# Kernel tuning notes

Measured on AMD Instinct MI355X. Metric: run time of the kernel, lower is better.

The kernel has to match this reference:

```python
import jax, jax.numpy as jnp
import numpy as np

K = 10
BN_EPS = 1e-5


def _edgeconv(x, W, b, gamma, beta):
    """DGCNN EdgeConv: kNN on x, edge feat [x_i, x_j - x_i], Linear->(BN)->ReLU, max over k.
    x: [N, C]; W: [2C, Cout]; gamma/beta: [Cout] or None."""
    sq = jnp.sum(x * x, axis=1)                      # [N]
    dist = sq[:, None] + sq[None, :] - 2.0 * (x @ x.T)  # [N, N] squared dists
    _, idx = jax.lax.top_k(-dist, K)                 # [N, K] (includes self)
    xj = x[idx]                                      # [N, K, C] gather
    xi = jnp.broadcast_to(x[:, None, :], xj.shape)   # [N, K, C]
    e = jnp.concatenate([xi, xj - xi], axis=-1)      # [N, K, 2C]
    h = e @ W + b                                    # [N, K, Cout]
    if gamma is not None:                            # BatchNorm1d (training-mode batch stats)
        mu = h.mean(axis=(0, 1))
        var = h.var(axis=(0, 1))
        h = (h - mu) * jax.lax.rsqrt(var + BN_EPS) * gamma + beta
    h = jax.nn.relu(h)
    return h.max(axis=1)                             # [N, Cout]


def _aggregate(f, seg_ids, num_segments):
    return jax.ops.segment_max(f, seg_ids, num_segments=num_segments)


def setup_inputs() -> dict:
    key = jax.random.key(0)
    ks = jax.random.split(key, 12)
    N, B = 16384, 64
    x = jax.random.normal(ks[0], (N, 3), dtype=jnp.float32)
    n_pts = jnp.full((B,), N // B, dtype=jnp.int32)

    def lin(k, fi, fo):
        s = 1.0 / np.sqrt(fi)
        kw, kb = jax.random.split(k)
        return (jax.random.uniform(kw, (fi, fo), jnp.float32, -s, s),
                jax.random.uniform(kb, (fo,), jnp.float32, -s, s))

    W1, b1 = lin(ks[1], 6, 64)
    W2, b2 = lin(ks[2], 128, 64)
    W3, b3 = lin(ks[3], 128, 64)
    W4, b4 = lin(ks[4], 128, 64)
    Wp, bp = lin(ks[5], 256, 128)
    g1 = jnp.ones((64,), jnp.float32); be1 = jnp.zeros((64,), jnp.float32)
    g3 = jnp.ones((64,), jnp.float32); be3 = jnp.zeros((64,), jnp.float32)
    return {"x": x, "n_pts": n_pts,
            "W1": W1, "b1": b1, "g1": g1, "be1": be1,
            "W2": W2, "b2": b2,
            "W3": W3, "b3": b3, "g3": g3, "be3": be3,
            "W4": W4, "b4": b4,
            "Wp": Wp, "bp": bp}


def reference(x, n_pts, W1, b1, g1, be1, W2, b2, W3, b3, g3, be3, W4, b4, Wp, bp):
    N = x.shape[0]
    B = n_pts.shape[0]
    seg_ids = jnp.repeat(jnp.arange(B, dtype=jnp.int32), n_pts, total_repeat_length=N)

    f1 = _edgeconv(x,  W1, b1, g1,  be1)   # [N, 64]
    f2 = _edgeconv(f1, W2, b2, None, None)
    f3 = _edgeconv(f2, W3, b3, g3,  be3)
    f4 = _edgeconv(f3, W4, b4, None, None)

    p = jnp.concatenate([_aggregate(f, seg_ids, B) for f in (f1, f2, f3, f4)], axis=1)  # [B, 256]
    f = jnp.tanh(p @ Wp + bp)              # [B, 128]
    f = f / (jnp.linalg.norm(f, axis=1, keepdims=True) + 1e-9)
    return f
```

## Files before the change

### kernel.cpp

```cpp
#include <hip/hip_runtime.h>
#include <hip/hip_bf16.h>

constexpr int N = 16384;
constexpr int KNN = 10;
constexpr int CF = 64;
constexpr int NS64 = 12;
constexpr int NS3 = 12;

#define FBIG 1e30f

typedef __attribute__((ext_vector_type(8))) __bf16 bfv8;
typedef __attribute__((ext_vector_type(4))) float f32x4;

#define TOPK_INSERT(dval, jval)                                            \
  if ((dval) < bmax) {                                                     \
    float mv = bd[0]; int slot = 0;                                        \
    _Pragma("unroll") for (int s_ = 1; s_ < 10; ++s_)                      \
      if (bd[s_] > mv) { mv = bd[s_]; slot = s_; }                         \
    _Pragma("unroll") for (int s_ = 0; s_ < 10; ++s_)                      \
      if (slot == s_) { bd[s_] = (dval); bi[s_] = (jval); }                \
    bmax = bd[0];                                                          \
    _Pragma("unroll") for (int s_ = 1; s_ < 10; ++s_)                      \
      bmax = fmaxf(bmax, bd[s_]);                                          \
  }

__device__ inline ushort bf16_rne(float x) {
  unsigned u = __float_as_uint(x);
  return (ushort)((u + 0x7FFFu + ((u >> 16) & 1u)) >> 16);
}
__device__ inline float bf16_to_f(ushort h) { return __uint_as_float(((unsigned)h) << 16); }

__global__ __launch_bounds__(256) void pack3_kernel(const float* __restrict__ X,
                                                    float4* __restrict__ xp,
                                                    int* __restrict__ gtauI,
                                                    float* __restrict__ accum) {
  int i = blockIdx.x * 256 + threadIdx.x;
  float x0 = X[3 * i], x1 = X[3 * i + 1], x2 = X[3 * i + 2];
  float s = fmaf(x0, x0, fmaf(x1, x1, x2 * x2));
  xp[i] = make_float4(x0, x1, x2, s);
  gtauI[i] = 0x7F7F7F7F;
  if (blockIdx.x == 0 && threadIdx.x < 128) accum[threadIdx.x] = 0.f;
}

__global__ __launch_bounds__(256) void prep128s_kernel(const float* __restrict__ X,
                                                       ushort* __restrict__ Xp,
                                                       float* __restrict__ sq,
                                                       int* __restrict__ gtauI,
                                                       float* __restrict__ accum) {
  int i = blockIdx.x * 256 + threadIdx.x;
  int n = i >> 4, k4 = (i & 15) << 2;
  float4 v = ((const float4*)X)[i];
  float vv[4] = {v.x, v.y, v.z, v.w};
  ushort h[4], lo[4];
#pragma unroll
  for (int k = 0; k < 4; ++k) {
    h[k] = bf16_rne(vv[k]);
    lo[k] = bf16_rne(vv[k] - bf16_to_f(h[k]));
  }
  ushort* row = Xp + (size_t)n * 128;
  *(ushort4*)(row + k4) = make_ushort4(h[0], h[1], h[2], h[3]);
  *(ushort4*)(row + 64 + k4) = make_ushort4(lo[0], lo[1], lo[2], lo[3]);
  float ps = fmaf(vv[0], vv[0], fmaf(vv[1], vv[1], fmaf(vv[2], vv[2], vv[3] * vv[3])));
#pragma unroll
  for (int m = 1; m < 16; m <<= 1) ps += __shfl_xor(ps, m, 16);
  if ((threadIdx.x & 15) == 0) {
    sq[n] = ps;
    gtauI[n] = 0x7F7F7F7F;
  }
  if (blockIdx.x == 0 && threadIdx.x < 128) accum[threadIdx.x] = 0.f;
}


__global__ __launch_bounds__(256, 3) void knn64w_kernel(const ushort* __restrict__ Xp,
                                                        const float* __restrict__ sq,
                                                        int* __restrict__ gtauI,
                                                        float* __restrict__ dpart,
                                                        ushort* __restrict__ ipart) {
  __shared__ float bufD[4][64 * 17];
  __shared__ ushort bufI[4][64 * 18];
  __shared__ __align__(16) float tauS[4][64];
  __shared__ int cntS[4][64];

  const int tid = threadIdx.x;
  const int w = tid >> 6, l = tid & 63, lp = l & 15, g = l >> 4;
  const int rg = blockIdx.x / NS64, cs = blockIdx.x % NS64;
  const int wbase = rg * 256 + w * 64;
  const int myrow = wbase + l;
  const int c0 = (1024 * cs) / NS64, c1 = (1024 * (cs + 1)) / NS64;

  tauS[w][l] = FBIG;
  cntS[w][l] = 0;
  __builtin_amdgcn_wave_barrier();

  bfv8 aH1[4], aH2[4], aL1[4], aL2[4];
#pragma unroll
  for (int rt = 0; rt < 4; ++rt) {
    const size_t ao = (size_t)(wbase + rt * 16 + lp) * 128 + g * 8;
    aH1[rt] = *(const bfv8*)&Xp[ao];
    aH2[rt] = *(const bfv8*)&Xp[ao + 32];
    aL1[rt] = *(const bfv8*)&Xp[ao + 64];
    aL2[rt] = *(const bfv8*)&Xp[ao + 96];
  }
  float sqi[16];
#pragma unroll
  for (int rt = 0; rt < 4; ++rt)
#pragma unroll
    for (int r = 0; r < 4; ++r) sqi[rt * 4 + r] = sq[wbase + rt * 16 + g * 4 + r];

  float bd[10]; int bi[10]; float bmax = FBIG; float lastPub = FBIG;
#pragma unroll
  for (int s = 0; s < 10; ++s) { bd[s] = FBIG; bi[s] = 0x7fffffff; }
  int gt = 0x7F7F7F7F;

  for (int t = c0; t < c1; ++t) {
    const int bcol = t * 16 + lp;
    const size_t bo = (size_t)bcol * 128 + g * 8;
    bfv8 bc0 = *(const bfv8*)&Xp[bo];
    bfv8 bc1 = *(const bfv8*)&Xp[bo + 32];
    bfv8 bc2 = *(const bfv8*)&Xp[bo + 64];
    bfv8 bc3 = *(const bfv8*)&Xp[bo + 96];
    float sjc = sq[bcol];
    int gtn = gtauI[myrow];

    __builtin_amdgcn_wave_barrier();
    {
      const int c = cntS[w][l];
      if (c) {
        const float* bD = &bufD[w][l * 17];
        const ushort* bI = &bufI[w][l * 18];
#pragma unroll 1
        for (int j = 0; j < c; ++j) {
          float d = bD[j];
          int ii = (int)bI[j];
          TOPK_INSERT(d, ii);
        }
        cntS[w][l] = 0;
      }
      tauS[w][l] = fminf(bmax, __int_as_float(gt));
      if (bmax < lastPub) {
        atomicMin(&gtauI[myrow], __float_as_int(bmax));
        lastPub = bmax;
      }
    }
    __builtin_amdgcn_wave_barrier();
    gt = gtn;

#pragma unroll
    for (int rt = 0; rt < 4; ++rt) {
      f32x4 acc = {0.f, 0.f, 0.f, 0.f};
      acc = __builtin_amdgcn_mfma_f32_16x16x32_bf16(aH1[rt], bc0, acc, 0, 0, 0);
      acc = __builtin_amdgcn_mfma_f32_16x16x32_bf16(aH2[rt], bc1, acc, 0, 0, 0);
      acc = __builtin_amdgcn_mfma_f32_16x16x32_bf16(aH1[rt], bc2, acc, 0, 0, 0);
      acc = __builtin_amdgcn_mfma_f32_16x16x32_bf16(aH2[rt], bc3, acc, 0, 0, 0);
      acc = __builtin_amdgcn_mfma_f32_16x16x32_bf16(aL1[rt], bc0, acc, 0, 0, 0);
      acc = __builtin_amdgcn_mfma_f32_16x16x32_bf16(aL2[rt], bc1, acc, 0, 0, 0);
      f32x4 taur = *(const f32x4*)&tauS[w][rt * 16 + g * 4];
#pragma unroll
      for (int r = 0; r < 4; ++r) {
        float d = fmaf(-2.f, acc[r], sqi[rt * 4 + r] + sjc);
        if (d < taur[r]) {
          int rloc = rt * 16 + g * 4 + r;
          int pos = atomicAdd(&cntS[w][rloc], 1);
          bufD[w][rloc * 17 + pos] = d;
          bufI[w][rloc * 18 + pos] = (ushort)bcol;
        }
      }
    }
  }

  __builtin_amdgcn_wave_barrier();
  {
    const int c = cntS[w][l];
    const float* bD = &bufD[w][l * 17];
    const ushort* bI = &bufI[w][l * 18];
#pragma unroll 1
    for (int j = 0; j < c; ++j) {
      float d = bD[j];
      int ii = (int)bI[j];
      TOPK_INSERT(d, ii);
    }
  }
  float* dp = dpart + ((size_t)cs * N + myrow) * 10;
  ushort* ip = ipart + ((size_t)cs * N + myrow) * 10;
#pragma unroll
  for (int s = 0; s < 10; ++s) { dp[s] = bd[s]; ip[s] = (ushort)bi[s]; }
}

__global__ __launch_bounds__(256, 3) void knn3g_kernel(const float4* __restrict__ xp,
                                                       int* __restrict__ gtauI,
                                                       float* __restrict__ dpart,
                                                       ushort* __restrict__ ipart) {
  __shared__ float bufD[4][64 * 17];
  __shared__ ushort bufI[4][64 * 18];
  __shared__ __align__(16) float tauS[4][64];
  __shared__ int cntS[4][64];

  const int tid = threadIdx.x;
  const int w = tid >> 6, l = tid & 63, lp = l & 15, g = l >> 4;
  const int rg = blockIdx.x / NS3, cs = blockIdx.x % NS3;
  const int wbase = rg * 256 + w * 64;
  const int myrow = wbase + l;
  const int c0 = (1024 * cs) / NS3, c1 = (1024 * (cs + 1)) / NS3;

  tauS[w][l] = FBIG;
  cntS[w][l] = 0;
  __builtin_amdgcn_wave_barrier();

  float4 rw[16];
#pragma unroll
  for (int rt = 0; rt < 4; ++rt)
#pragma unroll
    for (int r = 0; r < 4; ++r) rw[rt * 4 + r] = xp[wbase + rt * 16 + g * 4 + r];

  float bd[10]; int bi[10]; float bmax = FBIG; float lastPub = FBIG;
#pragma unroll
  for (int s = 0; s < 10; ++s) { bd[s] = FBIG; bi[s] = 0x7fffffff; }
  int gt = 0x7F7F7F7F;

  for (int t = c0; t < c1; ++t) {
    const int bcol = t * 16 + lp;
    const float4 oc = xp[bcol];
    int gtn = gtauI[myrow];

    __builtin_amdgcn_wave_barrier();
    {
      const int c = cntS[w][l];
      if (c) {
        const float* bD = &bufD[w][l * 17];
        const ushort* bI = &bufI[w][l * 18];
#pragma unroll 1
        for (int j = 0; j < c; ++j) {
          float d = bD[j];
          int ii = (int)bI[j];
          TOPK_INSERT(d, ii);
        }
        cntS[w][l] = 0;
      }
      tauS[w][l] = fminf(bmax, __int_as_float(gt));
      if (bmax < lastPub) {
        atomicMin(&gtauI[myrow], __float_as_int(bmax));
        lastPub = bmax;
      }
    }
    __builtin_amdgcn_wave_barrier();
    gt = gtn;

#pragma unroll
    for (int rt = 0; rt < 4; ++rt) {
      f32x4 taur = *(const f32x4*)&tauS[w][rt * 16 + g * 4];
#pragma unroll
      for (int r = 0; r < 4; ++r) {
        const float4 m = rw[rt * 4 + r];
        float dot = fmaf(m.x, oc.x, fmaf(m.y, oc.y, m.z * oc.z));
        float d = fmaf(-2.f, dot, m.w + oc.w);
        if (d < taur[r]) {
          int rloc = rt * 16 + g * 4 + r;
          int pos = atomicAdd(&cntS[w][rloc], 1);
          bufD[w][rloc * 17 + pos] = d;
          bufI[w][rloc * 18 + pos] = (ushort)bcol;
        }
      }
    }
  }

  __builtin_amdgcn_wave_barrier();
  {
    const int c = cntS[w][l];
    const float* bD = &bufD[w][l * 17];
    const ushort* bI = &bufI[w][l * 18];
#pragma unroll 1
    for (int j = 0; j < c; ++j) {
      float d = bD[j];
      int ii = (int)bI[j];
      TOPK_INSERT(d, ii);
    }
  }
  float* dp = dpart + ((size_t)cs * N + myrow) * 10;
  ushort* ip = ipart + ((size_t)cs * N + myrow) * 10;
#pragma unroll
  for (int s = 0; s < 10; ++s) { dp[s] = bd[s]; ip[s] = (ushort)bi[s]; }
}

template <int S>
__global__ __launch_bounds__(256) void merge_kernel(const float* __restrict__ dpart,
                                                    const ushort* __restrict__ ipart,
                                                    ushort* __restrict__ idx_out) {
  const int row = blockIdx.x * 256 + threadIdx.x;
  float d[S * 10]; int id_[S * 10];
#pragma unroll
  for (int p = 0; p < S; ++p)
#pragma unroll
    for (int s = 0; s < 10; ++s) {
      d[p * 10 + s] = dpart[((size_t)p * N + row) * 10 + s];
      id_[p * 10 + s] = (int)ipart[((size_t)p * N + row) * 10 + s];
    }
#pragma unroll
  for (int t = 0; t < 10; ++t) {
    float dm = d[0]; int im = id_[0]; int slot = 0;
#pragma unroll
    for (int e = 1; e < S * 10; ++e) {
      bool better = (d[e] < dm) || (d[e] == dm && id_[e] < im);
      if (better) { dm = d[e]; im = id_[e]; slot = e; }
    }
    idx_out[(size_t)row * 10 + t] = (ushort)im;
#pragma unroll
    for (int e = 0; e < S * 10; ++e)
      if (e == slot) d[e] = FBIG;
  }
}

__global__ __launch_bounds__(256) void uv_kernel(const float* __restrict__ Xf, int CIN,
                                                 const float* __restrict__ W,
                                                 const float* __restrict__ bias,
                                                 float* __restrict__ U, float* __restrict__ V) {
  int tid = threadIdx.x;
  int c = tid & 63, p = tid >> 6;
  int n = blockIdx.x * 4 + p;
  const float* xr = Xf + (size_t)n * CIN;
  float vt = 0.f, vb = 0.f;
  for (int m = 0; m < CIN; ++m) {
    float xm = xr[m];
    vt = fmaf(xm, W[m * 64 + c], vt);
    vb = fmaf(xm, W[(CIN + m) * 64 + c], vb);
  }
  U[(size_t)n * 64 + c] = vb;
  V[(size_t)n * 64 + c] = vt - vb + bias[c];
}

__global__ __launch_bounds__(256) void stats_kernel(const float* __restrict__ U,
                                                    const float* __restrict__ V,
                                                    const ushort* __restrict__ idx,
                                                    float* __restrict__ accum) {
  int tid = threadIdx.x;
  int c = tid & 63, p = tid >> 6;
  int base = blockIdx.x * 64;
  float s = 0.f, s2 = 0.f;
  for (int ch = 0; ch < 16; ++ch) {
    int n = base + ch * 4 + p;
    float vn = V[(size_t)n * 64 + c];
    const ushort* in_ = idx + (size_t)n * 10;
#pragma unroll
    for (int k = 0; k < 10; ++k) {
      float h = vn + U[(size_t)in_[k] * 64 + c];
      s += h;
      s2 = fmaf(h, h, s2);
    }
  }
  __shared__ float red[256], red2[256];
  red[tid] = s; red2[tid] = s2;
  __syncthreads();
  if (tid < 64) {
    float ts = red[tid] + red[64 + tid] + red[128 + tid] + red[192 + tid];
    float t2 = red2[tid] + red2[64 + tid] + red2[128 + tid] + red2[192 + tid];
    atomicAdd(&accum[tid], ts);
    atomicAdd(&accum[64 + tid], t2);
  }
}

__global__ void bnfin_kernel(const float* __restrict__ accum,
                             const float* __restrict__ gamma,
                             const float* __restrict__ beta,
                             float* __restrict__ scale, float* __restrict__ shift) {
  int c = threadIdx.x;
  float inv = 1.f / (float)(N * KNN);
  float mu = accum[c] * inv;
  float var = accum[64 + c] * inv - mu * mu;
  float sc = gamma[c] * rsqrtf(var + 1e-5f);
  scale[c] = sc;
  shift[c] = fmaf(-mu, sc, beta[c]);
}

__global__ __launch_bounds__(256) void apply_kernel(const float* __restrict__ U,
                                                    const float* __restrict__ V,
                                                    const ushort* __restrict__ idx,
                                                    const float* __restrict__ scale,
                                                    const float* __restrict__ shift,
                                                    int use_bn, float* __restrict__ Fout) {
  int tid = threadIdx.x;
  int c = tid & 63, p = tid >> 6;
  int n = blockIdx.x * 4 + p;
  float sc = use_bn ? scale[c] : 1.f;
  float sh = use_bn ? shift[c] : 0.f;
  float vn = V[(size_t)n * 64 + c];
  const ushort* in_ = idx + (size_t)n * 10;
  float m = 0.f;
#pragma unroll
  for (int k = 0; k < 10; ++k) {
    float h = vn + U[(size_t)in_[k] * 64 + c];
    m = fmaxf(m, fmaf(h, sc, sh));
  }
  Fout[(size_t)n * 64 + c] = m;
}

__global__ __launch_bounds__(256) void pool1_kernel(const float* __restrict__ f1,
                                                    const float* __restrict__ f2,
                                                    const float* __restrict__ f3,
                                                    const float* __restrict__ f4,
                                                    const int* __restrict__ n_pts,
                                                    float* __restrict__ Pp) {
  int b = blockIdx.x >> 2;
  int q = blockIdx.x & 3;
  int c = threadIdx.x;
  int off = 0;
  for (int i = 0; i < b; ++i) off += n_pts[i];
  int cnt_ = n_pts[b];
  int s0 = off + (cnt_ * q) / 4;
  int s1 = off + (cnt_ * (q + 1)) / 4;
  const float* f = (c < 64) ? f1 : (c < 128) ? f2 : (c < 192) ? f3 : f4;
  int ch = c & 63;
  float m = -3.4e38f;
  for (int t = s0; t < s1; ++t) m = fmaxf(m, f[(size_t)t * 64 + ch]);
  Pp[((size_t)q * 64 + b) * 256 + c] = m;
}

__global__ __launch_bounds__(128) void head_kernel(const float* __restrict__ Pp,
                                                   const float* __restrict__ Wp,
                                                   const float* __restrict__ bp,
                                                   float* __restrict__ out) {
  int b = blockIdx.x;
  int c = threadIdx.x;
  __shared__ float ps[256];
#pragma unroll
  for (int j = 0; j < 2; ++j) {
    int cc = c + j * 128;
    float m = Pp[(size_t)b * 256 + cc];
#pragma unroll
    for (int q = 1; q < 4; ++q) m = fmaxf(m, Pp[((size_t)q * 64 + b) * 256 + cc]);
    ps[cc] = m;
  }
  __syncthreads();
  float acc = bp[c];
  for (int m = 0; m < 256; ++m) acc = fmaf(ps[m], Wp[m * 128 + c], acc);
  float t = tanhf(acc);
  __shared__ float red[128];
  red[c] = t * t;
  __syncthreads();
  for (int s = 64; s > 0; s >>= 1) {
    if (c < s) red[c] += red[c + s];
    __syncthreads();
  }
  float nrm = sqrtf(red[0]);
  out[b * 128 + c] = t / (nrm + 1e-9f);
}

extern "C" void kernel_launch(void* const* d_in, const int* in_sizes, int n_in,
                              void* d_out, int out_size, void* d_ws, size_t ws_size,
                              hipStream_t stream) {
  const float* x = (const float*)d_in[0];
  const int* n_pts = (const int*)d_in[1];
  const float* W1 = (const float*)d_in[2];
  const float* b1 = (const float*)d_in[3];
  const float* g1 = (const float*)d_in[4];
  const float* be1 = (const float*)d_in[5];
  const float* W2 = (const float*)d_in[6];
  const float* b2 = (const float*)d_in[7];
  const float* W3 = (const float*)d_in[8];
  const float* b3 = (const float*)d_in[9];
  const float* g3 = (const float*)d_in[10];
  const float* be3 = (const float*)d_in[11];
  const float* W4 = (const float*)d_in[12];
  const float* b4 = (const float*)d_in[13];
  const float* Wp = (const float*)d_in[14];
  const float* bp = (const float*)d_in[15];
  float* out = (float*)d_out;

  char* w = (char*)d_ws;
  auto alloc = [&](size_t bytes) {
    char* p = w;
    w += (bytes + 255) & ~(size_t)255;
    return p;
  };
  const size_t FS = (size_t)N * 64 * 4;
  float* f1 = (float*)alloc(FS);
  float* f2 = (float*)alloc(FS);
  float* f3 = (float*)alloc(FS);
  float* f4 = (float*)alloc(FS);
  float* Ub = (float*)alloc(FS);
  float* dpartf = (float*)alloc((size_t)NS64 * N * 10 * 4);
  ushort* iparti = (ushort*)alloc((size_t)NS64 * N * 10 * 2);
  float4* xp = (float4*)alloc((size_t)N * 16);
  float* sqb = (float*)alloc((size_t)N * 4);
  int* gtauI = (int*)alloc((size_t)N * 4);
  ushort* idxb = (ushort*)alloc((size_t)N * 10 * 2);
  float* accum = (float*)alloc(512);
  float* scaleb = (float*)alloc(256);
  float* shiftb = (float*)alloc(256);
  float* Ppart = (float*)alloc((size_t)4 * 64 * 256 * 4);
  ushort* Xp128 = (ushort*)Ub;
  float* Vb = dpartf;
  (void)ws_size; (void)n_in; (void)in_sizes; (void)out_size;

  auto run_layer = [&](const float* fin, int cin, const float* W, const float* b,
                       const float* g, const float* be, int use_bn, float* fout) {
    if (cin == 3) {
      pack3_kernel<<<N / 256, 256, 0, stream>>>(fin, xp, gtauI, accum);
      knn3g_kernel<<<64 * NS3, 256, 0, stream>>>(xp, gtauI, dpartf, iparti);
      merge_kernel<NS3><<<N / 256, 256, 0, stream>>>(dpartf, iparti, idxb);
    } else {
      prep128s_kernel<<<N * 64 / 4 / 256, 256, 0, stream>>>(fin, Xp128, sqb, gtauI, accum);
      knn64w_kernel<<<64 * NS64, 256, 0, stream>>>(Xp128, sqb, gtauI, dpartf, iparti);
      merge_kernel<NS64><<<N / 256, 256, 0, stream>>>(dpartf, iparti, idxb);
    }
    uv_kernel<<<N / 4, 256, 0, stream>>>(fin, cin, W, b, Ub, Vb);
    if (use_bn) {
      stats_kernel<<<256, 256, 0, stream>>>(Ub, Vb, idxb, accum);
      bnfin_kernel<<<1, 64, 0, stream>>>(accum, g, be, scaleb, shiftb);
    }
    apply_kernel<<<N / 4, 256, 0, stream>>>(Ub, Vb, idxb, scaleb, shiftb, use_bn, fout);
  };

  run_layer(x, 3, W1, b1, g1, be1, 1, f1);
  run_layer(f1, 64, W2, b2, nullptr, nullptr, 0, f2);
  run_layer(f2, 64, W3, b3, g3, be3, 1, f3);
  run_layer(f3, 64, W4, b4, nullptr, nullptr, 0, f4);
  pool1_kernel<<<256, 256, 0, stream>>>(f1, f2, f3, f4, n_pts, Ppart);
  head_kernel<<<64, 128, 0, stream>>>(Ppart, Wp, bp, out);
}
```

Baseline: 1.355 ms.

## Process two column tiles per kNN iteration and stream the top-k merge

The kNN kernels now compute distances for 32 candidate columns per loop iteration instead of 16. This halves the number of per-iteration buffer drains, wave barriers and threshold updates, and gives the MFMA path two independent accumulator chains. The candidate buffers grow to 33/34 entries per row to hold the larger batch, which raises LDS use and may lower occupancy. The merge kernel now keeps a running top-10 in registers while streaming partial lists, replacing the selection over a full S*10 array, to reduce register pressure.

```diff
diff --git a/kernel.cpp b/kernel.cpp
--- a/kernel.cpp
+++ b/kernel.cpp
@@ -76,8 +76,8 @@
                                                         int* __restrict__ gtauI,
                                                         float* __restrict__ dpart,
                                                         ushort* __restrict__ ipart) {
-  __shared__ float bufD[4][64 * 17];
-  __shared__ ushort bufI[4][64 * 18];
+  __shared__ float bufD[4][64 * 33];
+  __shared__ ushort bufI[4][64 * 34];
   __shared__ __align__(16) float tauS[4][64];
   __shared__ int cntS[4][64];
 
@@ -86,7 +86,7 @@
   const int rg = blockIdx.x / NS64, cs = blockIdx.x % NS64;
   const int wbase = rg * 256 + w * 64;
   const int myrow = wbase + l;
-  const int c0 = (1024 * cs) / NS64, c1 = (1024 * (cs + 1)) / NS64;
+  const int c0 = (512 * cs) / NS64, c1 = (512 * (cs + 1)) / NS64;
 
   tauS[w][l] = FBIG;
   cntS[w][l] = 0;
@@ -113,21 +113,28 @@
   int gt = 0x7F7F7F7F;
 
   for (int t = c0; t < c1; ++t) {
-    const int bcol = t * 16 + lp;
-    const size_t bo = (size_t)bcol * 128 + g * 8;
-    bfv8 bc0 = *(const bfv8*)&Xp[bo];
-    bfv8 bc1 = *(const bfv8*)&Xp[bo + 32];
-    bfv8 bc2 = *(const bfv8*)&Xp[bo + 64];
-    bfv8 bc3 = *(const bfv8*)&Xp[bo + 96];
-    float sjc = sq[bcol];
+    const int col0 = t * 32 + lp;
+    const int col1 = col0 + 16;
+    const size_t bo0 = (size_t)col0 * 128 + g * 8;
+    bfv8 p0 = *(const bfv8*)&Xp[bo0];
+    bfv8 p1 = *(const bfv8*)&Xp[bo0 + 32];
+    bfv8 p2 = *(const bfv8*)&Xp[bo0 + 64];
+    bfv8 p3 = *(const bfv8*)&Xp[bo0 + 96];
+    const size_t bo1 = (size_t)col1 * 128 + g * 8;
+    bfv8 q0 = *(const bfv8*)&Xp[bo1];
+    bfv8 q1 = *(const bfv8*)&Xp[bo1 + 32];
+    bfv8 q2 = *(const bfv8*)&Xp[bo1 + 64];
+    bfv8 q3 = *(const bfv8*)&Xp[bo1 + 96];
+    float sj0 = sq[col0];
+    float sj1 = sq[col1];
     int gtn = gtauI[myrow];
 
     __builtin_amdgcn_wave_barrier();
     {
       const int c = cntS[w][l];
       if (c) {
-        const float* bD = &bufD[w][l * 17];
-        const ushort* bI = &bufI[w][l * 18];
+        const float* bD = &bufD[w][l * 33];
+        const ushort* bI = &bufI[w][l * 34];
 #pragma unroll 1
         for (int j = 0; j < c; ++j) {
           float d = bD[j];
@@ -147,22 +154,35 @@
 
 #pragma unroll
     for (int rt = 0; rt < 4; ++rt) {
-      f32x4 acc = {0.f, 0.f, 0.f, 0.f};
-      acc = __builtin_amdgcn_mfma_f32_16x16x32_bf16(aH1[rt], bc0, acc, 0, 0, 0);
-      acc = __builtin_amdgcn_mfma_f32_16x16x32_bf16(aH2[rt], bc1, acc, 0, 0, 0);
-      acc = __builtin_amdgcn_mfma_f32_16x16x32_bf16(aH1[rt], bc2, acc, 0, 0, 0);
-      acc = __builtin_amdgcn_mfma_f32_16x16x32_bf16(aH2[rt], bc3, acc, 0, 0, 0);
-      acc = __builtin_amdgcn_mfma_f32_16x16x32_bf16(aL1[rt], bc0, acc, 0, 0, 0);
-      acc = __builtin_amdgcn_mfma_f32_16x16x32_bf16(aL2[rt], bc1, acc, 0, 0, 0);
       f32x4 taur = *(const f32x4*)&tauS[w][rt * 16 + g * 4];
+      f32x4 acc0 = {0.f, 0.f, 0.f, 0.f};
+      acc0 = __builtin_amdgcn_mfma_f32_16x16x32_bf16(aH1[rt], p0, acc0, 0, 0, 0);
+      acc0 = __builtin_amdgcn_mfma_f32_16x16x32_bf16(aH2[rt], p1, acc0, 0, 0, 0);
+      acc0 = __builtin_amdgcn_mfma_f32_16x16x32_bf16(aH1[rt], p2, acc0, 0, 0, 0);
+      acc0 = __builtin_amdgcn_mfma_f32_16x16x32_bf16(aH2[rt], p3, acc0, 0, 0, 0);
+      acc0 = __builtin_amdgcn_mfma_f32_16x16x32_bf16(aL1[rt], p0, acc0, 0, 0, 0);
+      acc0 = __builtin_amdgcn_mfma_f32_16x16x32_bf16(aL2[rt], p1, acc0, 0, 0, 0);
+      f32x4 acc1 = {0.f, 0.f, 0.f, 0.f};
+      acc1 = __builtin_amdgcn_mfma_f32_16x16x32_bf16(aH1[rt], q0, acc1, 0, 0, 0);
+      acc1 = __builtin_amdgcn_mfma_f32_16x16x32_bf16(aH2[rt], q1, acc1, 0, 0, 0);
+      acc1 = __builtin_amdgcn_mfma_f32_16x16x32_bf16(aH1[rt], q2, acc1, 0, 0, 0);
+      acc1 = __builtin_amdgcn_mfma_f32_16x16x32_bf16(aH2[rt], q3, acc1, 0, 0, 0);
+      acc1 = __builtin_amdgcn_mfma_f32_16x16x32_bf16(aL1[rt], q0, acc1, 0, 0, 0);
+      acc1 = __builtin_amdgcn_mfma_f32_16x16x32_bf16(aL2[rt], q1, acc1, 0, 0, 0);
 #pragma unroll
       for (int r = 0; r < 4; ++r) {
-        float d = fmaf(-2.f, acc[r], sqi[rt * 4 + r] + sjc);
-        if (d < taur[r]) {
-          int rloc = rt * 16 + g * 4 + r;
+        const int rloc = rt * 16 + g * 4 + r;
+        float d0 = fmaf(-2.f, acc0[r], sqi[rt * 4 + r] + sj0);
+        if (d0 < taur[r]) {
           int pos = atomicAdd(&cntS[w][rloc], 1);
-          bufD[w][rloc * 17 + pos] = d;
-          bufI[w][rloc * 18 + pos] = (ushort)bcol;
+          bufD[w][rloc * 33 + pos] = d0;
+          bufI[w][rloc * 34 + pos] = (ushort)col0;
+        }
+        float d1 = fmaf(-2.f, acc1[r], sqi[rt * 4 + r] + sj1);
+        if (d1 < taur[r]) {
+          int pos = atomicAdd(&cntS[w][rloc], 1);
+          bufD[w][rloc * 33 + pos] = d1;
+          bufI[w][rloc * 34 + pos] = (ushort)col1;
         }
       }
     }
@@ -171,8 +191,8 @@
   __builtin_amdgcn_wave_barrier();
   {
     const int c = cntS[w][l];
-    const float* bD = &bufD[w][l * 17];
-    const ushort* bI = &bufI[w][l * 18];
+    const float* bD = &bufD[w][l * 33];
+    const ushort* bI = &bufI[w][l * 34];
 #pragma unroll 1
     for (int j = 0; j < c; ++j) {
       float d = bD[j];
@@ -190,8 +210,8 @@
                                                        int* __restrict__ gtauI,
                                                        float* __restrict__ dpart,
                                                        ushort* __restrict__ ipart) {
-  __shared__ float bufD[4][64 * 17];
-  __shared__ ushort bufI[4][64 * 18];
+  __shared__ float bufD[4][64 * 33];
+  __shared__ ushort bufI[4][64 * 34];
   __shared__ __align__(16) float tauS[4][64];
   __shared__ int cntS[4][64];
 
@@ -200,7 +220,7 @@
   const int rg = blockIdx.x / NS3, cs = blockIdx.x % NS3;
   const int wbase = rg * 256 + w * 64;
   const int myrow = wbase + l;
-  const int c0 = (1024 * cs) / NS3, c1 = (1024 * (cs + 1)) / NS3;
+  const int c0 = (512 * cs) / NS3, c1 = (512 * (cs + 1)) / NS3;
 
   tauS[w][l] = FBIG;
   cntS[w][l] = 0;
@@ -218,16 +238,18 @@
   int gt = 0x7F7F7F7F;
 
   for (int t = c0; t < c1; ++t) {
-    const int bcol = t * 16 + lp;
-    const float4 oc = xp[bcol];
+    const int col0 = t * 32 + lp;
+    const int col1 = col0 + 16;
+    const float4 oc0 = xp[col0];
+    const float4 oc1 = xp[col1];
     int gtn = gtauI[myrow];
 
     __builtin_amdgcn_wave_barrier();
     {
       const int c = cntS[w][l];
       if (c) {
-        const float* bD = &bufD[w][l * 17];
-        const ushort* bI = &bufI[w][l * 18];
+        const float* bD = &bufD[w][l * 33];
+        const ushort* bI = &bufI[w][l * 34];
 #pragma unroll 1
         for (int j = 0; j < c; ++j) {
           float d = bD[j];
@@ -251,13 +273,20 @@
 #pragma unroll
       for (int r = 0; r < 4; ++r) {
         const float4 m = rw[rt * 4 + r];
-        float dot = fmaf(m.x, oc.x, fmaf(m.y, oc.y, m.z * oc.z));
-        float d = fmaf(-2.f, dot, m.w + oc.w);
-        if (d < taur[r]) {
-          int rloc = rt * 16 + g * 4 + r;
+        const int rloc = rt * 16 + g * 4 + r;
+        float dot0 = fmaf(m.x, oc0.x, fmaf(m.y, oc0.y, m.z * oc0.z));
+        float d0 = fmaf(-2.f, dot0, m.w + oc0.w);
+        if (d0 < taur[r]) {
           int pos = atomicAdd(&cntS[w][rloc], 1);
-          bufD[w][rloc * 17 + pos] = d;
-          bufI[w][rloc * 18 + pos] = (ushort)bcol;
+          bufD[w][rloc * 33 + pos] = d0;
+          bufI[w][rloc * 34 + pos] = (ushort)col0;
+        }
+        float dot1 = fmaf(m.x, oc1.x, fmaf(m.y, oc1.y, m.z * oc1.z));
+        float d1 = fmaf(-2.f, dot1, m.w + oc1.w);
+        if (d1 < taur[r]) {
+          int pos = atomicAdd(&cntS[w][rloc], 1);
+          bufD[w][rloc * 33 + pos] = d1;
+          bufI[w][rloc * 34 + pos] = (ushort)col1;
         }
       }
     }
@@ -266,8 +295,8 @@
   __builtin_amdgcn_wave_barrier();
   {
     const int c = cntS[w][l];
-    const float* bD = &bufD[w][l * 17];
-    const ushort* bI = &bufI[w][l * 18];
+    const float* bD = &bufD[w][l * 33];
+    const ushort* bI = &bufI[w][l * 34];
 #pragma unroll 1
     for (int j = 0; j < c; ++j) {
       float d = bD[j];
@@ -286,26 +315,44 @@
                                                     const ushort* __restrict__ ipart,
                                                     ushort* __restrict__ idx_out) {
   const int row = blockIdx.x * 256 + threadIdx.x;
-  float d[S * 10]; int id_[S * 10];
-#pragma unroll
-  for (int p = 0; p < S; ++p)
+  float bd[10]; int bi[10];
+#pragma unroll
+  for (int s = 0; s < 10; ++s) { bd[s] = FBIG; bi[s] = 0x7fffffff; }
+  float wd = FBIG; int wi = 0x7fffffff;
+#pragma unroll 1
+  for (int p = 0; p < S; ++p) {
+    const float* dp = dpart + ((size_t)p * N + row) * 10;
+    const ushort* ip = ipart + ((size_t)p * N + row) * 10;
 #pragma unroll
     for (int s = 0; s < 10; ++s) {
-      d[p * 10 + s] = dpart[((size_t)p * N + row) * 10 + s];
-      id_[p * 10 + s] = (int)ipart[((size_t)p * N + row) * 10 + s];
-    }
-#pragma unroll
+      float d = dp[s];
+      int ii = (int)ip[s];
+      if (d < wd || (d == wd && ii < wi)) {
+        int slot = 0;
+        float md = bd[0]; int mi = bi[0];
+#pragma unroll
+        for (int e = 1; e < 10; ++e)
+          if (bd[e] > md || (bd[e] == md && bi[e] > mi)) { md = bd[e]; mi = bi[e]; slot = e; }
+#pragma unroll
+        for (int e = 0; e < 10; ++e)
+          if (e == slot) { bd[e] = d; bi[e] = ii; }
+        wd = bd[0]; wi = bi[0];
+#pragma unroll
+        for (int e = 1; e < 10; ++e)
+          if (bd[e] > wd || (bd[e] == wd && bi[e] > wi)) { wd = bd[e]; wi = bi[e]; }
+      }
+    }
+  }
+#pragma unroll 1
   for (int t = 0; t < 10; ++t) {
-    float dm = d[0]; int im = id_[0]; int slot = 0;
-#pragma unroll
-    for (int e = 1; e < S * 10; ++e) {
-      bool better = (d[e] < dm) || (d[e] == dm && id_[e] < im);
-      if (better) { dm = d[e]; im = id_[e]; slot = e; }
-    }
+    float dm = bd[0]; int im = bi[0]; int slot = 0;
+#pragma unroll
+    for (int e = 1; e < 10; ++e)
+      if (bd[e] < dm || (bd[e] == dm && bi[e] < im)) { dm = bd[e]; im = bi[e]; slot = e; }
     idx_out[(size_t)row * 10 + t] = (ushort)im;
 #pragma unroll
-    for (int e = 0; e < S * 10; ++e)
-      if (e == slot) d[e] = FBIG;
+    for (int e = 0; e < 10; ++e)
+      if (e == slot) bd[e] = FBIG;
   }
 }
 
```

Result: slower. 1.549 ms (+14.3%).
